# Kernel optimization log

Measured on AMD Instinct MI355X. Metric: run time of the kernel, lower is better.

## Reference

```python
import jax, jax.numpy as jnp
import numpy as np

RES, GATE, SKIP, K, DIL, CIN = 128, 256, 128, 3, 2, 80
PAD = (K - 1) * DIL


def _wn(v, g):
    # weight_norm: w = g * v / ||v||, norm over all dims except dim 0 (out_channels)
    norm = jnp.sqrt(jnp.sum(v * v, axis=(1, 2), keepdims=True))
    return v * (g.reshape(-1, 1, 1) / norm)


def setup_inputs() -> dict:
    key = jax.random.key(0)
    ks = jax.random.split(key, 12)
    s = lambda *sh: 1.0 / np.sqrt(np.prod(sh[1:]))
    d = {
        "x": jax.random.normal(ks[0], (8, RES, 32768), dtype=jnp.float32),
        "condition": jax.random.normal(ks[1], (8, CIN, 32768), dtype=jnp.float32),
        "conv_v": jax.random.normal(ks[2], (GATE, RES, K), dtype=jnp.float32) * s(GATE, RES, K),
        "conv_g": jnp.ones((GATE,), dtype=jnp.float32),
        "conv_b": jnp.zeros((GATE,), dtype=jnp.float32),
        "lc_v": jax.random.normal(ks[3], (GATE, CIN, 1), dtype=jnp.float32) * s(GATE, CIN, 1),
        "lc_g": jnp.ones((GATE,), dtype=jnp.float32),
        "skip_v": jax.random.normal(ks[4], (SKIP, GATE // 2, 1), dtype=jnp.float32) * s(SKIP, GATE // 2, 1),
        "skip_g": jnp.ones((SKIP,), dtype=jnp.float32),
        "skip_b": jnp.zeros((SKIP,), dtype=jnp.float32),
        "out_v": jax.random.normal(ks[5], (RES, GATE // 2, 1), dtype=jnp.float32) * s(RES, GATE // 2, 1),
        "out_g": jnp.ones((RES,), dtype=jnp.float32),
        "out_b": jnp.zeros((RES,), dtype=jnp.float32),
    }
    return d


def reference(x, condition, conv_v, conv_g, conv_b, lc_v, lc_g,
              skip_v, skip_g, skip_b, out_v, out_g, out_b):
    residual = x
    w = _wn(conv_v, conv_g)  # [GATE, RES, K]
    # torch pads symmetrically then slices [:, :, :-PAD]; equivalent to left-only pad
    h = jax.lax.conv_general_dilated(
        x, w, window_strides=(1,), padding=[(PAD, 0)], rhs_dilation=(DIL,),
        dimension_numbers=("NCH", "OIH", "NCH"))
    h = h + conv_b[None, :, None]  # [B, GATE, T]
    a, b = jnp.split(h, 2, axis=1)
    lc_w = _wn(lc_v, lc_g)[:, :, 0]  # [GATE, CIN]
    c = jnp.einsum("oc,bct->bot", lc_w, condition)
    ca, cb = jnp.split(c, 2, axis=1)
    g = jnp.tanh(a + ca) * jax.nn.sigmoid(b + cb)  # [B, GATE//2, T]
    skip_w = _wn(skip_v, skip_g)[:, :, 0]
    s = jnp.einsum("oc,bct->bot", skip_w, g) + skip_b[None, :, None]
    out_w = _wn(out_v, out_g)[:, :, 0]
    o = jnp.einsum("oc,bct->bot", out_w, g) + out_b[None, :, None]
    return (o + residual, s)
```

## Files before the change

### kernel.cpp

```cpp
#include <hip/hip_runtime.h>

#define B_N   8
#define T_N   32768
#define RESC  128
#define GATEC 256
#define CINC  80
#define CINP  96
#define NT    64
#define HALO  4
#define XROWS 68

#define XSTR_B 272
#define CSTR_B 208
#define CS_OFF 18496
#define LDS_BYTES (18496 + 13312)

#define AP1_ELEMS (16*12*512)
#define AP2_ELEMS (16*3*512)
#define AP3_ELEMS (16*4*512)

#define OFF_S ((size_t)B_N * RESC * T_N)

typedef __attribute__((ext_vector_type(8))) short short8;
typedef __attribute__((ext_vector_type(4))) float f32x4;

__device__ __forceinline__ ushort f2bf(float f) {
  union { float f; unsigned int u; } c; c.f = f;
  unsigned int u = c.u;
  u += 0x7fffu + ((u >> 16) & 1u);
  return (ushort)(u >> 16);
}

__device__ __forceinline__ char* lds_at(char* base, int row, int strB, int colB) {
  int off = row * strB + colB;
  off ^= ((row >> 3) & 7) << 4;
  return base + off;
}

__global__ __launch_bounds__(256) void wn_pack_kernel(
    const float* __restrict__ conv_v, const float* __restrict__ conv_g,
    const float* __restrict__ lc_v,  const float* __restrict__ lc_g,
    const float* __restrict__ skip_v,const float* __restrict__ skip_g,
    const float* __restrict__ out_v, const float* __restrict__ out_g,
    ushort* __restrict__ Ap1, ushort* __restrict__ Ap2, ushort* __restrict__ Ap3) {
  const int o   = blockIdx.x;
  const int tid = threadIdx.x;
  const int mtg = o >> 4, r = o & 15;
  __shared__ float red[256];

  float s = 0.f;
  for (int e = tid; e < RESC * 3; e += 256) { float v = conv_v[o * RESC * 3 + e]; s += v * v; }
  red[tid] = s; __syncthreads();
  for (int off = 128; off > 0; off >>= 1) { if (tid < off) red[tid] += red[tid + off]; __syncthreads(); }
  const float csc = conv_g[o] / sqrtf(red[0]);
  __syncthreads();
  for (int e = tid; e < 384; e += 256) {
    const int ks = e >> 5, q = (e >> 3) & 3, j = e & 7;
    const int tap = ks >> 2, ci = (ks & 3) * 32 + q * 8 + j;
    Ap1[((mtg * 12 + ks) * 64 + q * 16 + r) * 8 + j] = f2bf(conv_v[(o * RESC + ci) * 3 + tap] * csc);
  }

  s = 0.f;
  for (int e = tid; e < CINC; e += 256) { float v = lc_v[o * CINC + e]; s += v * v; }
  red[tid] = s; __syncthreads();
  for (int off = 128; off > 0; off >>= 1) { if (tid < off) red[tid] += red[tid + off]; __syncthreads(); }
  const float lsc = lc_g[o] / sqrtf(red[0]);
  __syncthreads();
  for (int e = tid; e < CINP; e += 256) {
    const int ks = e >> 5, q = (e >> 3) & 3, j = e & 7;
    const float wv = (e < CINC) ? lc_v[o * CINC + e] * lsc : 0.f;
    Ap2[((mtg * 3 + ks) * 64 + q * 16 + r) * 8 + j] = f2bf(wv);
  }

  const float* vrow = (o < 128) ? (skip_v + o * 128) : (out_v + (o - 128) * 128);
  const float  gg   = (o < 128) ? skip_g[o] : out_g[o - 128];
  s = 0.f;
  for (int e = tid; e < 128; e += 256) { float v = vrow[e]; s += v * v; }
  red[tid] = s; __syncthreads();
  for (int off = 128; off > 0; off >>= 1) { if (tid < off) red[tid] += red[tid + off]; __syncthreads(); }
  const float ssc = gg / sqrtf(red[0]);
  for (int e = tid; e < 128; e += 256) {
    const int ks = e >> 5, q = (e >> 3) & 3, j = e & 7;
    Ap3[((mtg * 4 + ks) * 64 + q * 16 + r) * 8 + j] = f2bf(vrow[e] * ssc);
  }
}

__global__ __launch_bounds__(256) void fused_block_kernel(
    const float* __restrict__ x, const float* __restrict__ cond,
    const float* __restrict__ conv_b, const float* __restrict__ skip_b,
    const float* __restrict__ out_b,
    const ushort* __restrict__ Ap1, const ushort* __restrict__ Ap2,
    const ushort* __restrict__ Ap3,
    float* __restrict__ out) {
  const int tid  = threadIdx.x;
  const int w    = tid >> 6;
  const int lane = tid & 63;
  const int q    = lane >> 4;
  const int n    = lane & 15;
  const int blk  = blockIdx.x;
  const int b    = blk >> 9;
  const int t0   = (blk & 511) << 6;

  __shared__ __align__(128) char smem[LDS_BYTES];
  char* xs = smem;
  char* cs = smem + CS_OFF;
  char* gs = smem;

  {
    const int g4 = tid >> 3;
    const int c0 = g4 << 2;
    const int tt = (tid & 7) << 3;
    const float* xp = x + ((size_t)b * RESC + c0) * T_N + t0 + tt;
    float va[4][8];
#pragma unroll
    for (int rr = 0; rr < 4; ++rr) {
      const float4* rp = (const float4*)(xp + (size_t)rr * T_N);
      const float4 a0 = rp[0], a1 = rp[1];
      va[rr][0] = a0.x; va[rr][1] = a0.y; va[rr][2] = a0.z; va[rr][3] = a0.w;
      va[rr][4] = a1.x; va[rr][5] = a1.y; va[rr][6] = a1.z; va[rr][7] = a1.w;
    }
#pragma unroll
    for (int ss = 0; ss < 8; ++ss) {
      const unsigned lo = (unsigned)f2bf(va[0][ss]) | ((unsigned)f2bf(va[1][ss]) << 16);
      const unsigned hi = (unsigned)f2bf(va[2][ss]) | ((unsigned)f2bf(va[3][ss]) << 16);
      *(uint2*)lds_at(xs, HALO + tt + ss, XSTR_B, c0 * 2) = make_uint2(lo, hi);
    }
  }
  if (tid < RESC) {
    float h0 = 0.f, h1 = 0.f, h2 = 0.f, h3 = 0.f;
    if (t0 > 0) {
      const float4 hv = *(const float4*)(x + ((size_t)b * RESC + tid) * T_N + t0 - 4);
      h0 = hv.x; h1 = hv.y; h2 = hv.z; h3 = hv.w;
    }
    *(ushort*)lds_at(xs, 0, XSTR_B, tid * 2) = f2bf(h0);
    *(ushort*)lds_at(xs, 1, XSTR_B, tid * 2) = f2bf(h1);
    *(ushort*)lds_at(xs, 2, XSTR_B, tid * 2) = f2bf(h2);
    *(ushort*)lds_at(xs, 3, XSTR_B, tid * 2) = f2bf(h3);
  }
  if (tid < 160) {
    const int g4 = tid >> 3;
    const int c0 = g4 << 2;
    const int tt = (tid & 7) << 3;
    const float* cp = cond + ((size_t)b * CINC + c0) * T_N + t0 + tt;
    float va[4][8];
#pragma unroll
    for (int rr = 0; rr < 4; ++rr) {
      const float4* rp = (const float4*)(cp + (size_t)rr * T_N);
      const float4 a0 = rp[0], a1 = rp[1];
      va[rr][0] = a0.x; va[rr][1] = a0.y; va[rr][2] = a0.z; va[rr][3] = a0.w;
      va[rr][4] = a1.x; va[rr][5] = a1.y; va[rr][6] = a1.z; va[rr][7] = a1.w;
    }
#pragma unroll
    for (int ss = 0; ss < 8; ++ss) {
      const unsigned lo = (unsigned)f2bf(va[0][ss]) | ((unsigned)f2bf(va[1][ss]) << 16);
      const unsigned hi = (unsigned)f2bf(va[2][ss]) | ((unsigned)f2bf(va[3][ss]) << 16);
      *(uint2*)lds_at(cs, tt + ss, CSTR_B, c0 * 2) = make_uint2(lo, hi);
    }
  } else {
    const int e0 = tid - 160;
    for (int z = e0; z < 512; z += 96) {
      const int row = z >> 3, c = z & 7;
      *(unsigned int*)lds_at(cs, row, CSTR_B, 160 + c * 4) = 0u;
    }
  }
  __syncthreads();

  const int mtile[4] = {2 * w, 2 * w + 1, 8 + 2 * w, 9 + 2 * w};
  f32x4 acc[4][4];
#pragma unroll
  for (int mt = 0; mt < 4; ++mt) {
    const float4 cb = *(const float4*)(conv_b + mtile[mt] * 16 + q * 4);
#pragma unroll
    for (int nt = 0; nt < 4; ++nt) acc[mt][nt] = (f32x4){cb.x, cb.y, cb.z, cb.w};
  }
#pragma unroll
  for (int ks = 0; ks < 12; ++ks) {
    const int tap = ks >> 2;
    const int cbyte = ((ks & 3) << 6);
    short8 af[4], bfr[4];
#pragma unroll
    for (int mt = 0; mt < 4; ++mt)
      af[mt] = *(const short8*)(Ap1 + ((mtile[mt] * 12 + ks) * 64 + lane) * 8);
#pragma unroll
    for (int nt = 0; nt < 4; ++nt)
      bfr[nt] = *(const short8*)lds_at(xs, nt * 16 + n + tap * 2, XSTR_B, cbyte + q * 16);
#pragma unroll
    for (int mt = 0; mt < 4; ++mt)
#pragma unroll
      for (int nt = 0; nt < 4; ++nt)
        acc[mt][nt] = __builtin_amdgcn_mfma_f32_16x16x32_bf16(af[mt], bfr[nt], acc[mt][nt], 0, 0, 0);
  }
#pragma unroll
  for (int ks = 0; ks < 3; ++ks) {
    short8 af[4], bfr[4];
#pragma unroll
    for (int mt = 0; mt < 4; ++mt)
      af[mt] = *(const short8*)(Ap2 + ((mtile[mt] * 3 + ks) * 64 + lane) * 8);
#pragma unroll
    for (int nt = 0; nt < 4; ++nt)
      bfr[nt] = *(const short8*)lds_at(cs, nt * 16 + n, CSTR_B, ks * 64 + q * 16);
#pragma unroll
    for (int mt = 0; mt < 4; ++mt)
#pragma unroll
      for (int nt = 0; nt < 4; ++nt)
        acc[mt][nt] = __builtin_amdgcn_mfma_f32_16x16x32_bf16(af[mt], bfr[nt], acc[mt][nt], 0, 0, 0);
  }
  __syncthreads();

#pragma unroll
  for (int mt = 0; mt < 2; ++mt)
#pragma unroll
    for (int nt = 0; nt < 4; ++nt) {
      const f32x4 va = acc[mt][nt];
      const f32x4 vb = acc[mt + 2][nt];
      float r[4];
#pragma unroll
      for (int i = 0; i < 4; ++i) {
        const float ta = 1.f - 2.f / (__expf(2.f * va[i]) + 1.f);
        const float sb = 1.f / (1.f + __expf(-vb[i]));
        r[i] = ta * sb;
      }
      const unsigned lo = (unsigned)f2bf(r[0]) | ((unsigned)f2bf(r[1]) << 16);
      const unsigned hi = (unsigned)f2bf(r[2]) | ((unsigned)f2bf(r[3]) << 16);
      *(uint2*)lds_at(gs, nt * 16 + n, XSTR_B, 64 * w + 32 * mt + 8 * q) = make_uint2(lo, hi);
    }
  __syncthreads();

  const int colbase = (w & 1) << 6;
  {
    const float* bias = (w < 2) ? skip_b : out_b;
#pragma unroll
    for (int mt = 0; mt < 4; ++mt) {
      const float4 bb = *(const float4*)(bias + colbase + mt * 16 + q * 4);
#pragma unroll
      for (int nt = 0; nt < 4; ++nt) acc[mt][nt] = (f32x4){bb.x, bb.y, bb.z, bb.w};
    }
#pragma unroll
    for (int ks = 0; ks < 4; ++ks) {
      short8 af[4], bfr[4];
#pragma unroll
      for (int mt = 0; mt < 4; ++mt)
        af[mt] = *(const short8*)(Ap3 + ((w * 4 + mt) * 4 + ks) * 512 + lane * 8);
#pragma unroll
      for (int nt = 0; nt < 4; ++nt)
        bfr[nt] = *(const short8*)lds_at(gs, nt * 16 + n, XSTR_B, ks * 64 + q * 16);
#pragma unroll
      for (int mt = 0; mt < 4; ++mt)
#pragma unroll
        for (int nt = 0; nt < 4; ++nt)
          acc[mt][nt] = __builtin_amdgcn_mfma_f32_16x16x32_bf16(af[mt], bfr[nt], acc[mt][nt], 0, 0, 0);
    }
  }

#pragma unroll
  for (int mt = 0; mt < 4; ++mt)
#pragma unroll
    for (int nt = 0; nt < 4; ++nt) {
      const int ch = colbase + mt * 16 + q * 4;
      const int t  = t0 + nt * 16 + n;
      const f32x4 v = acc[mt][nt];
      if (w < 2) {
        float* dst = out + OFF_S + ((size_t)(b * RESC + ch)) * T_N + t;
#pragma unroll
        for (int i = 0; i < 4; ++i) dst[(size_t)i * T_N] = v[i];
      } else {
        const float* xr = x + ((size_t)(b * RESC + ch)) * T_N + t;
        float* dst = out + ((size_t)(b * RESC + ch)) * T_N + t;
#pragma unroll
        for (int i = 0; i < 4; ++i) dst[(size_t)i * T_N] = v[i] + xr[(size_t)i * T_N];
      }
    }
}

extern "C" void kernel_launch(void* const* d_in, const int* in_sizes, int n_in,
                              void* d_out, int out_size, void* d_ws, size_t ws_size,
                              hipStream_t stream) {
  const float* x      = (const float*)d_in[0];
  const float* cond   = (const float*)d_in[1];
  const float* conv_v = (const float*)d_in[2];
  const float* conv_g = (const float*)d_in[3];
  const float* conv_b = (const float*)d_in[4];
  const float* lc_v   = (const float*)d_in[5];
  const float* lc_g   = (const float*)d_in[6];
  const float* skip_v = (const float*)d_in[7];
  const float* skip_g = (const float*)d_in[8];
  const float* skip_b = (const float*)d_in[9];
  const float* out_v  = (const float*)d_in[10];
  const float* out_g  = (const float*)d_in[11];
  const float* out_b  = (const float*)d_in[12];

  ushort* Ap1 = (ushort*)d_ws;
  ushort* Ap2 = Ap1 + AP1_ELEMS;
  ushort* Ap3 = Ap2 + AP2_ELEMS;

  hipLaunchKernelGGL(wn_pack_kernel, dim3(256), dim3(256), 0, stream,
                     conv_v, conv_g, lc_v, lc_g, skip_v, skip_g, out_v, out_g,
                     Ap1, Ap2, Ap3);
  hipLaunchKernelGGL(fused_block_kernel, dim3(4096), dim3(256), 0, stream,
                     x, cond, conv_b, skip_b, out_b, Ap1, Ap2, Ap3, (float*)d_out);
}
```

Measured before the change: 543.3 us.

## Double block to 512 threads, split output tiles across eight waves

Launches the fused kernel with 512 threads (8 waves) instead of 256. Each wave now owns one tanh tile and one sigmoid tile instead of two of each, halving per-wave accumulators and MFMA work. The input loads for x, condition and halo are spread over dedicated thread groups, removing serialized branches. In the output stage every wave computes matching skip and out channels, so each wave writes both outputs. This aims to raise latency hiding and occupancy through lower register pressure, at the cost of more A-fragment loads per block and more barrier participants.

```diff
diff --git a/kernel.cpp b/kernel.cpp
--- a/kernel.cpp
+++ b/kernel.cpp
@@ -85,7 +85,7 @@
   }
 }
 
-__global__ __launch_bounds__(256) void fused_block_kernel(
+__global__ __launch_bounds__(512) void fused_block_kernel(
     const float* __restrict__ x, const float* __restrict__ cond,
     const float* __restrict__ conv_b, const float* __restrict__ skip_b,
     const float* __restrict__ out_b,
@@ -106,9 +106,8 @@
   char* cs = smem + CS_OFF;
   char* gs = smem;
 
-  {
-    const int g4 = tid >> 3;
-    const int c0 = g4 << 2;
+  if (tid < 256) {
+    const int c0 = (tid >> 3) << 2;
     const int tt = (tid & 7) << 3;
     const float* xp = x + ((size_t)b * RESC + c0) * T_N + t0 + tt;
     float va[4][8];
@@ -125,151 +124,147 @@
       const unsigned hi = (unsigned)f2bf(va[2][ss]) | ((unsigned)f2bf(va[3][ss]) << 16);
       *(uint2*)lds_at(xs, HALO + tt + ss, XSTR_B, c0 * 2) = make_uint2(lo, hi);
     }
-  }
-  if (tid < RESC) {
-    float h0 = 0.f, h1 = 0.f, h2 = 0.f, h3 = 0.f;
+  } else if (tid < 448) {
+    const int e  = tid - 256;
+    const int c0 = (e >> 3) << 2;
+    const int tt = (e & 7) << 3;
+    if (c0 < CINC) {
+      const float* cp = cond + ((size_t)b * CINC + c0) * T_N + t0 + tt;
+      float va[4][8];
+#pragma unroll
+      for (int rr = 0; rr < 4; ++rr) {
+        const float4* rp = (const float4*)(cp + (size_t)rr * T_N);
+        const float4 a0 = rp[0], a1 = rp[1];
+        va[rr][0] = a0.x; va[rr][1] = a0.y; va[rr][2] = a0.z; va[rr][3] = a0.w;
+        va[rr][4] = a1.x; va[rr][5] = a1.y; va[rr][6] = a1.z; va[rr][7] = a1.w;
+      }
+#pragma unroll
+      for (int ss = 0; ss < 8; ++ss) {
+        const unsigned lo = (unsigned)f2bf(va[0][ss]) | ((unsigned)f2bf(va[1][ss]) << 16);
+        const unsigned hi = (unsigned)f2bf(va[2][ss]) | ((unsigned)f2bf(va[3][ss]) << 16);
+        *(uint2*)lds_at(cs, tt + ss, CSTR_B, c0 * 2) = make_uint2(lo, hi);
+      }
+    } else {
+#pragma unroll
+      for (int ss = 0; ss < 8; ++ss)
+        *(uint2*)lds_at(cs, tt + ss, CSTR_B, c0 * 2) = make_uint2(0u, 0u);
+    }
+  } else {
+    const int e   = tid - 448;
+    const int ch0 = e << 1;
+    float h0[4] = {0.f, 0.f, 0.f, 0.f}, h1[4] = {0.f, 0.f, 0.f, 0.f};
     if (t0 > 0) {
-      const float4 hv = *(const float4*)(x + ((size_t)b * RESC + tid) * T_N + t0 - 4);
-      h0 = hv.x; h1 = hv.y; h2 = hv.z; h3 = hv.w;
-    }
-    *(ushort*)lds_at(xs, 0, XSTR_B, tid * 2) = f2bf(h0);
-    *(ushort*)lds_at(xs, 1, XSTR_B, tid * 2) = f2bf(h1);
-    *(ushort*)lds_at(xs, 2, XSTR_B, tid * 2) = f2bf(h2);
-    *(ushort*)lds_at(xs, 3, XSTR_B, tid * 2) = f2bf(h3);
-  }
-  if (tid < 160) {
-    const int g4 = tid >> 3;
-    const int c0 = g4 << 2;
-    const int tt = (tid & 7) << 3;
-    const float* cp = cond + ((size_t)b * CINC + c0) * T_N + t0 + tt;
-    float va[4][8];
+      const float4 v0 = *(const float4*)(x + ((size_t)b * RESC + ch0) * T_N + t0 - 4);
+      const float4 v1 = *(const float4*)(x + ((size_t)b * RESC + ch0 + 1) * T_N + t0 - 4);
+      h0[0] = v0.x; h0[1] = v0.y; h0[2] = v0.z; h0[3] = v0.w;
+      h1[0] = v1.x; h1[1] = v1.y; h1[2] = v1.z; h1[3] = v1.w;
+    }
 #pragma unroll
     for (int rr = 0; rr < 4; ++rr) {
-      const float4* rp = (const float4*)(cp + (size_t)rr * T_N);
-      const float4 a0 = rp[0], a1 = rp[1];
-      va[rr][0] = a0.x; va[rr][1] = a0.y; va[rr][2] = a0.z; va[rr][3] = a0.w;
-      va[rr][4] = a1.x; va[rr][5] = a1.y; va[rr][6] = a1.z; va[rr][7] = a1.w;
-    }
-#pragma unroll
-    for (int ss = 0; ss < 8; ++ss) {
-      const unsigned lo = (unsigned)f2bf(va[0][ss]) | ((unsigned)f2bf(va[1][ss]) << 16);
-      const unsigned hi = (unsigned)f2bf(va[2][ss]) | ((unsigned)f2bf(va[3][ss]) << 16);
-      *(uint2*)lds_at(cs, tt + ss, CSTR_B, c0 * 2) = make_uint2(lo, hi);
-    }
-  } else {
-    const int e0 = tid - 160;
-    for (int z = e0; z < 512; z += 96) {
-      const int row = z >> 3, c = z & 7;
-      *(unsigned int*)lds_at(cs, row, CSTR_B, 160 + c * 4) = 0u;
-    }
-  }
-  __syncthreads();
-
-  const int mtile[4] = {2 * w, 2 * w + 1, 8 + 2 * w, 9 + 2 * w};
-  f32x4 acc[4][4];
-#pragma unroll
-  for (int mt = 0; mt < 4; ++mt) {
-    const float4 cb = *(const float4*)(conv_b + mtile[mt] * 16 + q * 4);
-#pragma unroll
-    for (int nt = 0; nt < 4; ++nt) acc[mt][nt] = (f32x4){cb.x, cb.y, cb.z, cb.w};
+      const unsigned pk = (unsigned)f2bf(h0[rr]) | ((unsigned)f2bf(h1[rr]) << 16);
+      *(unsigned int*)lds_at(xs, rr, XSTR_B, ch0 * 2) = pk;
+    }
+  }
+  __syncthreads();
+
+  const int mtA = w, mtB = 8 + w;
+  f32x4 acc[2][4];
+  {
+    const float4 ca = *(const float4*)(conv_b + mtA * 16 + q * 4);
+    const float4 cb = *(const float4*)(conv_b + mtB * 16 + q * 4);
+#pragma unroll
+    for (int nt = 0; nt < 4; ++nt) {
+      acc[0][nt] = (f32x4){ca.x, ca.y, ca.z, ca.w};
+      acc[1][nt] = (f32x4){cb.x, cb.y, cb.z, cb.w};
+    }
   }
 #pragma unroll
   for (int ks = 0; ks < 12; ++ks) {
     const int tap = ks >> 2;
     const int cbyte = ((ks & 3) << 6);
-    short8 af[4], bfr[4];
-#pragma unroll
-    for (int mt = 0; mt < 4; ++mt)
-      af[mt] = *(const short8*)(Ap1 + ((mtile[mt] * 12 + ks) * 64 + lane) * 8);
+    const short8 af0 = *(const short8*)(Ap1 + ((mtA * 12 + ks) * 64 + lane) * 8);
+    const short8 af1 = *(const short8*)(Ap1 + ((mtB * 12 + ks) * 64 + lane) * 8);
+    short8 bfr[4];
 #pragma unroll
     for (int nt = 0; nt < 4; ++nt)
       bfr[nt] = *(const short8*)lds_at(xs, nt * 16 + n + tap * 2, XSTR_B, cbyte + q * 16);
 #pragma unroll
-    for (int mt = 0; mt < 4; ++mt)
-#pragma unroll
-      for (int nt = 0; nt < 4; ++nt)
-        acc[mt][nt] = __builtin_amdgcn_mfma_f32_16x16x32_bf16(af[mt], bfr[nt], acc[mt][nt], 0, 0, 0);
+    for (int nt = 0; nt < 4; ++nt) {
+      acc[0][nt] = __builtin_amdgcn_mfma_f32_16x16x32_bf16(af0, bfr[nt], acc[0][nt], 0, 0, 0);
+      acc[1][nt] = __builtin_amdgcn_mfma_f32_16x16x32_bf16(af1, bfr[nt], acc[1][nt], 0, 0, 0);
+    }
   }
 #pragma unroll
   for (int ks = 0; ks < 3; ++ks) {
-    short8 af[4], bfr[4];
-#pragma unroll
-    for (int mt = 0; mt < 4; ++mt)
-      af[mt] = *(const short8*)(Ap2 + ((mtile[mt] * 3 + ks) * 64 + lane) * 8);
+    const short8 af0 = *(const short8*)(Ap2 + ((mtA * 3 + ks) * 64 + lane) * 8);
+    const short8 af1 = *(const short8*)(Ap2 + ((mtB * 3 + ks) * 64 + lane) * 8);
+    short8 bfr[4];
 #pragma unroll
     for (int nt = 0; nt < 4; ++nt)
       bfr[nt] = *(const short8*)lds_at(cs, nt * 16 + n, CSTR_B, ks * 64 + q * 16);
 #pragma unroll
-    for (int mt = 0; mt < 4; ++mt)
-#pragma unroll
-      for (int nt = 0; nt < 4; ++nt)
-        acc[mt][nt] = __builtin_amdgcn_mfma_f32_16x16x32_bf16(af[mt], bfr[nt], acc[mt][nt], 0, 0, 0);
-  }
-  __syncthreads();
-
-#pragma unroll
-  for (int mt = 0; mt < 2; ++mt)
-#pragma unroll
-    for (int nt = 0; nt < 4; ++nt) {
-      const f32x4 va = acc[mt][nt];
-      const f32x4 vb = acc[mt + 2][nt];
-      float r[4];
-#pragma unroll
-      for (int i = 0; i < 4; ++i) {
-        const float ta = 1.f - 2.f / (__expf(2.f * va[i]) + 1.f);
-        const float sb = 1.f / (1.f + __expf(-vb[i]));
-        r[i] = ta * sb;
-      }
-      const unsigned lo = (unsigned)f2bf(r[0]) | ((unsigned)f2bf(r[1]) << 16);
-      const unsigned hi = (unsigned)f2bf(r[2]) | ((unsigned)f2bf(r[3]) << 16);
-      *(uint2*)lds_at(gs, nt * 16 + n, XSTR_B, 64 * w + 32 * mt + 8 * q) = make_uint2(lo, hi);
-    }
-  __syncthreads();
-
-  const int colbase = (w & 1) << 6;
+    for (int nt = 0; nt < 4; ++nt) {
+      acc[0][nt] = __builtin_amdgcn_mfma_f32_16x16x32_bf16(af0, bfr[nt], acc[0][nt], 0, 0, 0);
+      acc[1][nt] = __builtin_amdgcn_mfma_f32_16x16x32_bf16(af1, bfr[nt], acc[1][nt], 0, 0, 0);
+    }
+  }
+  __syncthreads();
+
+#pragma unroll
+  for (int nt = 0; nt < 4; ++nt) {
+    const f32x4 va = acc[0][nt];
+    const f32x4 vb = acc[1][nt];
+    float r[4];
+#pragma unroll
+    for (int i = 0; i < 4; ++i) {
+      const float ta = 1.f - 2.f / (__expf(2.f * va[i]) + 1.f);
+      const float sb = 1.f / (1.f + __expf(-vb[i]));
+      r[i] = ta * sb;
+    }
+    const unsigned lo = (unsigned)f2bf(r[0]) | ((unsigned)f2bf(r[1]) << 16);
+    const unsigned hi = (unsigned)f2bf(r[2]) | ((unsigned)f2bf(r[3]) << 16);
+    *(uint2*)lds_at(gs, nt * 16 + n, XSTR_B, (16 * w + 4 * q) * 2) = make_uint2(lo, hi);
+  }
+  __syncthreads();
+
   {
-    const float* bias = (w < 2) ? skip_b : out_b;
-#pragma unroll
-    for (int mt = 0; mt < 4; ++mt) {
-      const float4 bb = *(const float4*)(bias + colbase + mt * 16 + q * 4);
-#pragma unroll
-      for (int nt = 0; nt < 4; ++nt) acc[mt][nt] = (f32x4){bb.x, bb.y, bb.z, bb.w};
-    }
-#pragma unroll
-    for (int ks = 0; ks < 4; ++ks) {
-      short8 af[4], bfr[4];
-#pragma unroll
-      for (int mt = 0; mt < 4; ++mt)
-        af[mt] = *(const short8*)(Ap3 + ((w * 4 + mt) * 4 + ks) * 512 + lane * 8);
-#pragma unroll
-      for (int nt = 0; nt < 4; ++nt)
-        bfr[nt] = *(const short8*)lds_at(gs, nt * 16 + n, XSTR_B, ks * 64 + q * 16);
-#pragma unroll
-      for (int mt = 0; mt < 4; ++mt)
-#pragma unroll
-        for (int nt = 0; nt < 4; ++nt)
-          acc[mt][nt] = __builtin_amdgcn_mfma_f32_16x16x32_bf16(af[mt], bfr[nt], acc[mt][nt], 0, 0, 0);
-    }
-  }
-
-#pragma unroll
-  for (int mt = 0; mt < 4; ++mt)
-#pragma unroll
-    for (int nt = 0; nt < 4; ++nt) {
-      const int ch = colbase + mt * 16 + q * 4;
-      const int t  = t0 + nt * 16 + n;
-      const f32x4 v = acc[mt][nt];
-      if (w < 2) {
-        float* dst = out + OFF_S + ((size_t)(b * RESC + ch)) * T_N + t;
-#pragma unroll
-        for (int i = 0; i < 4; ++i) dst[(size_t)i * T_N] = v[i];
-      } else {
-        const float* xr = x + ((size_t)(b * RESC + ch)) * T_N + t;
-        float* dst = out + ((size_t)(b * RESC + ch)) * T_N + t;
-#pragma unroll
-        for (int i = 0; i < 4; ++i) dst[(size_t)i * T_N] = v[i] + xr[(size_t)i * T_N];
-      }
-    }
+    const float4 bs = *(const float4*)(skip_b + w * 16 + q * 4);
+    const float4 bo = *(const float4*)(out_b  + w * 16 + q * 4);
+#pragma unroll
+    for (int nt = 0; nt < 4; ++nt) {
+      acc[0][nt] = (f32x4){bs.x, bs.y, bs.z, bs.w};
+      acc[1][nt] = (f32x4){bo.x, bo.y, bo.z, bo.w};
+    }
+  }
+#pragma unroll
+  for (int ks = 0; ks < 4; ++ks) {
+    const short8 af0 = *(const short8*)(Ap3 + ((w * 4 + ks) * 64 + lane) * 8);
+    const short8 af1 = *(const short8*)(Ap3 + (((8 + w) * 4 + ks) * 64 + lane) * 8);
+    short8 bfr[4];
+#pragma unroll
+    for (int nt = 0; nt < 4; ++nt)
+      bfr[nt] = *(const short8*)lds_at(gs, nt * 16 + n, XSTR_B, ks * 64 + q * 16);
+#pragma unroll
+    for (int nt = 0; nt < 4; ++nt) {
+      acc[0][nt] = __builtin_amdgcn_mfma_f32_16x16x32_bf16(af0, bfr[nt], acc[0][nt], 0, 0, 0);
+      acc[1][nt] = __builtin_amdgcn_mfma_f32_16x16x32_bf16(af1, bfr[nt], acc[1][nt], 0, 0, 0);
+    }
+  }
+
+  const int ch = 16 * w + 4 * q;
+#pragma unroll
+  for (int nt = 0; nt < 4; ++nt) {
+    const int t = t0 + nt * 16 + n;
+    const f32x4 vs = acc[0][nt];
+    const f32x4 vo = acc[1][nt];
+    float* ds = out + OFF_S + ((size_t)(b * RESC + ch)) * T_N + t;
+#pragma unroll
+    for (int i = 0; i < 4; ++i) ds[(size_t)i * T_N] = vs[i];
+    const float* xr = x + ((size_t)(b * RESC + ch)) * T_N + t;
+    float* dо = out + ((size_t)(b * RESC + ch)) * T_N + t;
+#pragma unroll
+    for (int i = 0; i < 4; ++i) dо[(size_t)i * T_N] = vo[i] + xr[(size_t)i * T_N];
+  }
 }
 
 extern "C" void kernel_launch(void* const* d_in, const int* in_sizes, int n_in,
@@ -296,6 +291,6 @@
   hipLaunchKernelGGL(wn_pack_kernel, dim3(256), dim3(256), 0, stream,
                      conv_v, conv_g, lc_v, lc_g, skip_v, skip_g, out_v, out_g,
                      Ap1, Ap2, Ap3);
-  hipLaunchKernelGGL(fused_block_kernel, dim3(4096), dim3(256), 0, stream,
+  hipLaunchKernelGGL(fused_block_kernel, dim3(4096), dim3(512), 0, stream,
                      x, cond, conv_b, skip_b, out_b, Ap1, Ap2, Ap3, (float*)d_out);
 }
```

Measured after the change: 504.2 us. -7.2%, faster.
